# Optimization experiments

Hardware: AMD Instinct MI355X
Metric: run time of the kernel (lower is better)

The kernel has to match this reference:

```python
import jax, jax.numpy as jnp
import numpy as np

N = 100000
E = 3200000
NFEAT, NHID, NCLASS = 256, 128, 40


def setup_inputs() -> dict:
    key = jax.random.key(0)
    ks = jax.random.split(key, 8)
    return {
        "x": jax.random.normal(ks[0], (N, NFEAT), dtype=jnp.float32),
        "edge_src": jax.random.randint(ks[1], (E,), 0, N, dtype=jnp.int32),
        "edge_dst": jax.random.randint(ks[2], (E,), 0, N, dtype=jnp.int32),
        "edge_w": jax.random.uniform(ks[3], (E,), dtype=jnp.float32),
        "W0": jax.random.normal(ks[4], (NFEAT, NHID), dtype=jnp.float32) * (2.0 / (NFEAT + NHID)) ** 0.5,
        "b0": jax.random.normal(ks[5], (1, NHID), dtype=jnp.float32) * 0.1,
        "W1": jax.random.normal(ks[6], (NHID, NCLASS), dtype=jnp.float32) * (2.0 / (NHID + NCLASS)) ** 0.5,
        "b1": jax.random.normal(ks[7], (1, NCLASS), dtype=jnp.float32) * 0.1,
    }


def _l2_normalize(h, eps=1e-12):
    # F.normalize(x, p=2, dim=1)
    nrm = jnp.sqrt(jnp.sum(h * h, axis=1, keepdims=True))
    return h / jnp.maximum(nrm, eps)


def reference(x, edge_src, edge_dst, edge_w, W0, b0, W1, b1):
    n_nodes = x.shape[0]

    def spmm(h):  # adj @ h with edge-list sparse adjacency
        return jax.ops.segment_sum(edge_w[:, None] * h[edge_src], edge_dst, num_segments=n_nodes)

    # layer 1: GraphConvolution = spmm(x @ W) + bias (dropout is identity in eval)
    h = spmm(x @ W0) + b0
    h = _l2_normalize(h)        # atg.Z1
    h = jax.nn.relu(h)          # atg.H1
    # layer 2
    z = spmm(h @ W1) + b1       # atg.Z2
    return jax.nn.log_softmax(z, axis=1)
```

## Files before the change

### kernel.cpp

```cpp
#include <hip/hip_runtime.h>
#include <math.h>

#define NN 100000
#define NE 3200000
#define NF 256
#define NH 128
#define NC 40

#define CH 8192
#define NBLK 391
#define NBUCK 782
#define HTOT (NBUCK * NBLK)
#define HS1 ((HTOT + 511) / 512)
#define NTILE 1563

typedef unsigned int uint;
typedef short short8 __attribute__((ext_vector_type(8)));
typedef float floatx4 __attribute__((ext_vector_type(4)));

__device__ __forceinline__ float bflo(uint v) { return __uint_as_float(v << 16); }
__device__ __forceinline__ float bfhi(uint v) { return __uint_as_float(v & 0xffff0000u); }
__device__ __forceinline__ unsigned short f2bf(float f) {
    const uint u = __float_as_uint(f);
    return (unsigned short)((u + 0x7fffu + ((u >> 16) & 1u)) >> 16);
}
__device__ __forceinline__ uint pack2bf(float a, float b) {
    return (uint)f2bf(a) | ((uint)f2bf(b) << 16);
}

union ABfrag { uint u[4]; short8 s; };

__global__ __launch_bounds__(256) void w0pack_k(const float* __restrict__ W0,
                                                uint4* __restrict__ W0p) {
    const int idx = blockIdx.x * 256 + threadIdx.x;
    if (idx >= 4096) return;
    const int lane  = idx & 63;
    const int ntile = (idx >> 6) & 7;
    const int kstep = idx >> 9;
    const int n  = ntile * 16 + (lane & 15);
    const int kb = kstep * 32 + (lane >> 4) * 8;
    uint w[4];
#pragma unroll
    for (int ww = 0; ww < 4; ++ww)
        w[ww] = pack2bf(W0[(size_t)(kb + 2 * ww) * NH + n],
                        W0[(size_t)(kb + 2 * ww + 1) * NH + n]);
    W0p[idx] = make_uint4(w[0], w[1], w[2], w[3]);
}

__global__ __launch_bounds__(256) void gemm1_mfma(const float* __restrict__ x,
                                                  const uint4* __restrict__ W0p,
                                                  unsigned short* __restrict__ xwh) {
    __shared__ __align__(16) uint4 sB[4096];
    for (int i = threadIdx.x; i < 4096; i += 256) sB[i] = W0p[i];
    __syncthreads();

    const int wave = threadIdx.x >> 6;
    const int lane = threadIdx.x & 63;
    const int quad = lane >> 4;
    const int mcol = lane & 15;

    for (int tile = blockIdx.x; tile < NTILE; tile += 512) {
        const int row  = tile * 64 + wave * 16 + mcol;
        const int rowc = min(row, NN - 1);
        const float* xr = x + (size_t)rowc * NF + quad * 8;

        floatx4 acc[8] = {};
        float4 lo = *(const float4*)(xr);
        float4 hi = *(const float4*)(xr + 4);
#pragma unroll
        for (int ks = 0; ks < 8; ++ks) {
            ABfrag a;
            a.u[0] = pack2bf(lo.x, lo.y);
            a.u[1] = pack2bf(lo.z, lo.w);
            a.u[2] = pack2bf(hi.x, hi.y);
            a.u[3] = pack2bf(hi.z, hi.w);
            if (ks < 7) {
                lo = *(const float4*)(xr + (ks + 1) * 32);
                hi = *(const float4*)(xr + (ks + 1) * 32 + 4);
            }
#pragma unroll
            for (int nt = 0; nt < 8; ++nt) {
                ABfrag b;
                const uint4 bw = sB[(ks * 8 + nt) * 64 + lane];
                b.u[0] = bw.x; b.u[1] = bw.y; b.u[2] = bw.z; b.u[3] = bw.w;
                acc[nt] = __builtin_amdgcn_mfma_f32_16x16x32_bf16(a.s, b.s, acc[nt], 0, 0, 0);
            }
        }
        const int rowbase = tile * 64 + wave * 16 + quad * 4;
#pragma unroll
        for (int nt = 0; nt < 8; ++nt) {
#pragma unroll
            for (int r = 0; r < 4; ++r) {
                const int rr = rowbase + r;
                if (rr < NN) xwh[(size_t)rr * NH + nt * 16 + mcol] = f2bf(acc[nt][r]);
            }
        }
    }
}

__global__ __launch_bounds__(256) void p1hist_k(const int* __restrict__ edst,
                                                int* __restrict__ hmat) {
    __shared__ uint h[NBUCK];
    for (int i = threadIdx.x; i < NBUCK; i += 256) h[i] = 0;
    __syncthreads();
    const int b = blockIdx.x;
    const int e0 = b * CH, e1 = min(NE, e0 + CH);
    for (int e = e0 + threadIdx.x; e < e1; e += 256)
        atomicAdd(&h[((uint)edst[e]) >> 7], 1u);
    __syncthreads();
    for (int i = threadIdx.x; i < NBUCK; i += 256)
        hmat[(size_t)i * NBLK + b] = (int)h[i];
}

__global__ __launch_bounds__(512) void hscan1_k(int* __restrict__ hmat,
                                                int* __restrict__ partials) {
    __shared__ int s[512];
    const int t = threadIdx.x;
    const int i = blockIdx.x * 512 + t;
    const int v = (i < HTOT) ? hmat[i] : 0;
    s[t] = v;
    __syncthreads();
#pragma unroll
    for (int off = 1; off < 512; off <<= 1) {
        int a = (t >= off) ? s[t - off] : 0;
        __syncthreads();
        s[t] += a;
        __syncthreads();
    }
    if (i < HTOT) hmat[i] = s[t] - v;
    if (t == 511) partials[blockIdx.x] = s[t];
}

__global__ __launch_bounds__(1024) void hscan2_k(int* __restrict__ partials, int nb) {
    __shared__ int s[1024];
    const int t = threadIdx.x;
    const int v = (t < nb) ? partials[t] : 0;
    s[t] = v;
    __syncthreads();
#pragma unroll
    for (int off = 1; off < 1024; off <<= 1) {
        int a = (t >= off) ? s[t - off] : 0;
        __syncthreads();
        s[t] += a;
        __syncthreads();
    }
    if (t < nb) partials[t] = s[t] - v;
}

__global__ __launch_bounds__(512) void hscan3_k(int* __restrict__ hmat,
                                                const int* __restrict__ partials) {
    const int i = blockIdx.x * 512 + threadIdx.x;
    if (i < HTOT) hmat[i] += partials[blockIdx.x];
}

__global__ __launch_bounds__(256) void p1scat_k(const int* __restrict__ esrc,
                                                const int* __restrict__ edst,
                                                const float* __restrict__ ew,
                                                const int* __restrict__ hmat,
                                                uint2* __restrict__ ep1) {
    __shared__ uint base[NBUCK];
    const int b = blockIdx.x;
    for (int i = threadIdx.x; i < NBUCK; i += 256)
        base[i] = (uint)hmat[(size_t)i * NBLK + b];
    __syncthreads();
    const int e0 = b * CH, e1 = min(NE, e0 + CH);
    for (int e = e0 + threadIdx.x; e < e1; e += 256) {
        const uint d = (uint)edst[e];
        const uint pos = atomicAdd(&base[d >> 7], 1u);
        ep1[pos] = make_uint2((uint)esrc[e] | ((d & 127u) << 17), __float_as_uint(ew[e]));
    }
}

__global__ __launch_bounds__(256) void p2_k(const int* __restrict__ hmat,
                                            const uint2* __restrict__ ep1,
                                            uint2* __restrict__ ep,
                                            int* __restrict__ rp) {
    const int bk = blockIdx.x;
    const int beg = hmat[(size_t)bk * NBLK];
    const int end = (bk == NBUCK - 1) ? NE : hmat[(size_t)(bk + 1) * NBLK];
    __shared__ uint cnt[128];
    __shared__ uint st[128];
    if (threadIdx.x < 128) cnt[threadIdx.x] = 0;
    __syncthreads();
    for (int j = beg + threadIdx.x; j < end; j += 256)
        atomicAdd(&cnt[(ep1[j].x >> 17) & 127u], 1u);
    __syncthreads();
    if (threadIdx.x < 128) st[threadIdx.x] = cnt[threadIdx.x];
    __syncthreads();
#pragma unroll
    for (int off = 1; off < 128; off <<= 1) {
        uint a = 0;
        if (threadIdx.x < 128 && threadIdx.x >= off) a = st[threadIdx.x - off];
        __syncthreads();
        if (threadIdx.x < 128) st[threadIdx.x] += a;
        __syncthreads();
    }
    if (threadIdx.x < 128) {
        const uint start = st[threadIdx.x] - cnt[threadIdx.x];
        const int d = bk * 128 + threadIdx.x;
        if (d < NN) rp[d] = beg + (int)start;
        cnt[threadIdx.x] = (uint)beg + start;
    }
    if (bk == 0 && threadIdx.x == 200) rp[NN] = NE;
    __syncthreads();
    for (int j = beg + threadIdx.x; j < end; j += 256) {
        const uint2 r = ep1[j];
        const uint pos = atomicAdd(&cnt[(r.x >> 17) & 127u], 1u);
        ep[pos] = r;
    }
}

__global__ __launch_bounds__(256) void spmm1n_g(const int* __restrict__ rp,
                                                const uint2* __restrict__ ep,
                                                const uint* __restrict__ xwb,
                                                const float* __restrict__ b0,
                                                uint* __restrict__ h2b) {
    const int n = blockIdx.x * 4 + (threadIdx.x >> 6);
    const int t = threadIdx.x & 63;
    const int beg = rp[n], end = rp[n + 1];
    float a0 = 0.f, a1 = 0.f;
    int j = beg;
    for (; j + 7 < end; j += 8) {
        uint2 e[8];
        uint v[8];
#pragma unroll
        for (int u = 0; u < 8; ++u) e[u] = ep[j + u];
#pragma unroll
        for (int u = 0; u < 8; ++u) v[u] = xwb[(size_t)(e[u].x & 0x1FFFFu) * 64 + t];
#pragma unroll
        for (int u = 0; u < 8; ++u) {
            const float w = __uint_as_float(e[u].y);
            a0 = fmaf(w, bflo(v[u]), a0);
            a1 = fmaf(w, bfhi(v[u]), a1);
        }
    }
    for (; j < end; ++j) {
        const uint2 e = ep[j];
        const uint v = xwb[(size_t)(e.x & 0x1FFFFu) * 64 + t];
        const float w = __uint_as_float(e.y);
        a0 = fmaf(w, bflo(v), a0); a1 = fmaf(w, bfhi(v), a1);
    }
    const float2 bb = *(const float2*)(b0 + 2 * t);
    const float v0 = a0 + bb.x, v1 = a1 + bb.y;
    float s = v0 * v0 + v1 * v1;
#pragma unroll
    for (int o = 1; o < 64; o <<= 1) s += __shfl_xor(s, o, 64);
    const float scale = 1.0f / fmaxf(sqrtf(s), 1e-12f);
    h2b[(size_t)n * 64 + t] = pack2bf(fmaxf(v0 * scale, 0.0f), fmaxf(v1 * scale, 0.0f));
}

__global__ void gemm2_k(const uint* __restrict__ h2b,
                        const float* __restrict__ W1,
                        unsigned short* __restrict__ hwh) {
    __shared__ float sW1[NH * NC];
    const int lt = threadIdx.y * NC + threadIdx.x;
    for (int i = lt; i < NH * NC; i += 240) sW1[i] = W1[i];
    __syncthreads();
    const int n = blockIdx.x * 6 + threadIdx.y;
    if (n >= NN) return;
    const int f = threadIdx.x;
    const uint* hr = h2b + (size_t)n * 64;
    float acc = 0.f;
#pragma unroll 4
    for (int k8 = 0; k8 < 16; ++k8) {
        const uint4 hv = *(const uint4*)(hr + k8 * 4);
        const int kb = k8 * 8;
        acc = fmaf(bflo(hv.x), sW1[(kb + 0) * NC + f], acc);
        acc = fmaf(bfhi(hv.x), sW1[(kb + 1) * NC + f], acc);
        acc = fmaf(bflo(hv.y), sW1[(kb + 2) * NC + f], acc);
        acc = fmaf(bfhi(hv.y), sW1[(kb + 3) * NC + f], acc);
        acc = fmaf(bflo(hv.z), sW1[(kb + 4) * NC + f], acc);
        acc = fmaf(bfhi(hv.z), sW1[(kb + 5) * NC + f], acc);
        acc = fmaf(bflo(hv.w), sW1[(kb + 6) * NC + f], acc);
        acc = fmaf(bfhi(hv.w), sW1[(kb + 7) * NC + f], acc);
    }
    hwh[(size_t)n * NC + f] = f2bf(acc);
}

__global__ __launch_bounds__(320) void spmm2l_g(const int* __restrict__ rp,
                                                const uint2* __restrict__ ep,
                                                const uint* __restrict__ hwb,
                                                const float* __restrict__ b1,
                                                float2* __restrict__ out2) {
    const int nl = threadIdx.x / 20;
    const int g  = threadIdx.x % 20;
    const int n  = blockIdx.x * 16 + nl;
    const int beg = rp[n], end = rp[n + 1];
    float a0 = 0.f, a1 = 0.f;
    int j = beg;
    for (; j + 7 < end; j += 8) {
        uint2 e[8];
        uint v[8];
#pragma unroll
        for (int u = 0; u < 8; ++u) e[u] = ep[j + u];
#pragma unroll
        for (int u = 0; u < 8; ++u) v[u] = hwb[(size_t)(e[u].x & 0x1FFFFu) * 20 + g];
#pragma unroll
        for (int u = 0; u < 8; ++u) {
            const float w = __uint_as_float(e[u].y);
            a0 = fmaf(w, bflo(v[u]), a0);
            a1 = fmaf(w, bfhi(v[u]), a1);
        }
    }
    for (; j < end; ++j) {
        const uint2 e = ep[j];
        const uint v = hwb[(size_t)(e.x & 0x1FFFFu) * 20 + g];
        const float w = __uint_as_float(e.y);
        a0 = fmaf(w, bflo(v), a0); a1 = fmaf(w, bfhi(v), a1);
    }
    const float2 bb = *(const float2*)(b1 + 2 * g);
    a0 += bb.x; a1 += bb.y;
    __shared__ float red[16 * 20];
    __shared__ float stat[16];
    red[nl * 20 + g] = fmaxf(a0, a1);
    __syncthreads();
    if (g == 0) {
        float m = -INFINITY;
#pragma unroll
        for (int q = 0; q < 20; ++q) m = fmaxf(m, red[nl * 20 + q]);
        stat[nl] = m;
    }
    __syncthreads();
    const float m = stat[nl];
    red[nl * 20 + g] = expf(a0 - m) + expf(a1 - m);
    __syncthreads();
    if (g == 0) {
        float ssum = 0.f;
#pragma unroll
        for (int q = 0; q < 20; ++q) ssum += red[nl * 20 + q];
        stat[nl] = logf(ssum);
    }
    __syncthreads();
    const float lse = stat[nl];
    out2[(size_t)n * 20 + g] = make_float2(a0 - m - lse, a1 - m - lse);
}

extern "C" void kernel_launch(void* const* d_in, const int* in_sizes, int n_in,
                              void* d_out, int out_size, void* d_ws, size_t ws_size,
                              hipStream_t stream) {
    const float* x    = (const float*)d_in[0];
    const int*   esrc = (const int*)d_in[1];
    const int*   edst = (const int*)d_in[2];
    const float* ew   = (const float*)d_in[3];
    const float* W0   = (const float*)d_in[4];
    const float* b0   = (const float*)d_in[5];
    const float* W1   = (const float*)d_in[6];
    const float* b1   = (const float*)d_in[7];
    float* out = (float*)d_out;

    size_t o = 0;
    uint*  xwb  = (uint*)d_ws + o;  o += (size_t)NN * 64;
    uint*  h2b  = (uint*)d_ws + o;  o += (size_t)NN * 64;
    uint2* ep1  = (uint2*)h2b;
    uint*  hwb  = (uint*)d_ws + o;  o += (size_t)NN * 20;
    uint2* ep   = (uint2*)((uint*)d_ws + o); o += (size_t)NE * 2;
    int*   hmat = (int*)d_ws + o;   o += HTOT;
    int*   rp   = (int*)d_ws + o;   o += NN + 2;
    int*   partials = (int*)d_ws + o; o += 1024;
    if (o & 3) o += 4 - (o & 3);
    uint4* W0p  = (uint4*)((uint*)d_ws + o); o += 16384;

    w0pack_k<<<16, 256, 0, stream>>>(W0, W0p);
    gemm1_mfma<<<512, 256, 0, stream>>>(x, W0p, (unsigned short*)xwb);

    p1hist_k<<<NBLK, 256, 0, stream>>>(edst, hmat);
    hscan1_k<<<HS1, 512, 0, stream>>>(hmat, partials);
    hscan2_k<<<1, 1024, 0, stream>>>(partials, HS1);
    hscan3_k<<<HS1, 512, 0, stream>>>(hmat, partials);
    p1scat_k<<<NBLK, 256, 0, stream>>>(esrc, edst, ew, hmat, ep1);
    p2_k<<<NBUCK, 256, 0, stream>>>(hmat, ep1, ep, rp);

    spmm1n_g<<<NN / 4, 256, 0, stream>>>(rp, ep, xwb, b0, h2b);
    gemm2_k<<<(NN + 5) / 6, dim3(40, 6), 0, stream>>>(h2b, W1, (unsigned short*)hwb);
    spmm2l_g<<<NN / 16, 320, 0, stream>>>(rp, ep, hwb, b1, (float2*)out);
}
```

Measured before the change: 580.4 us.

## Use MFMA for second GEMM, fold scan fixup, vectorize histogram, scalarize edge loads

Replaces the scalar FMA gemm2 with a bf16 MFMA kernel that uses a W1 panel pre-packed and zero-padded to 48 columns, with the packing fused into the W0 pack kernel. Drops the hscan3 fixup kernel and instead adds the block partials directly where p1scat and p2 read hmat. Vectorizes the histogram edge loads to int4. In spmm1 it broadcasts the edge src and weight through readfirstlane so they sit in scalar registers. Together these cut kernel launches, ALU work and VGPR pressure. The int4 histogram loop assumes the chunk size divides evenly, which holds for CH=8192 and NE.

```diff
diff --git a/kernel.cpp b/kernel.cpp
--- a/kernel.cpp
+++ b/kernel.cpp
@@ -30,21 +30,39 @@
 
 union ABfrag { uint u[4]; short8 s; };
 
-__global__ __launch_bounds__(256) void w0pack_k(const float* __restrict__ W0,
-                                                uint4* __restrict__ W0p) {
+__global__ __launch_bounds__(256) void prep_pack_k(const float* __restrict__ W0,
+                                                   const float* __restrict__ W1,
+                                                   uint4* __restrict__ W0p,
+                                                   uint4* __restrict__ W1p) {
     const int idx = blockIdx.x * 256 + threadIdx.x;
-    if (idx >= 4096) return;
-    const int lane  = idx & 63;
-    const int ntile = (idx >> 6) & 7;
-    const int kstep = idx >> 9;
-    const int n  = ntile * 16 + (lane & 15);
-    const int kb = kstep * 32 + (lane >> 4) * 8;
-    uint w[4];
-#pragma unroll
-    for (int ww = 0; ww < 4; ++ww)
-        w[ww] = pack2bf(W0[(size_t)(kb + 2 * ww) * NH + n],
-                        W0[(size_t)(kb + 2 * ww + 1) * NH + n]);
-    W0p[idx] = make_uint4(w[0], w[1], w[2], w[3]);
+    if (idx < 4096) {
+        const int lane  = idx & 63;
+        const int ntile = (idx >> 6) & 7;
+        const int kstep = idx >> 9;
+        const int n  = ntile * 16 + (lane & 15);
+        const int kb = kstep * 32 + (lane >> 4) * 8;
+        uint w[4];
+#pragma unroll
+        for (int ww = 0; ww < 4; ++ww)
+            w[ww] = pack2bf(W0[(size_t)(kb + 2 * ww) * NH + n],
+                            W0[(size_t)(kb + 2 * ww + 1) * NH + n]);
+        W0p[idx] = make_uint4(w[0], w[1], w[2], w[3]);
+    } else if (idx < 4096 + 768) {
+        const int i2 = idx - 4096;
+        const int lane  = i2 & 63;
+        const int ntile = (i2 >> 6) % 3;
+        const int kstep = (i2 >> 6) / 3;
+        const int n  = ntile * 16 + (lane & 15);
+        const int kb = kstep * 32 + (lane >> 4) * 8;
+        uint w[4];
+#pragma unroll
+        for (int ww = 0; ww < 4; ++ww) {
+            const float lo = (n < NC) ? W1[(size_t)(kb + 2 * ww) * NC + n] : 0.0f;
+            const float hi = (n < NC) ? W1[(size_t)(kb + 2 * ww + 1) * NC + n] : 0.0f;
+            w[ww] = pack2bf(lo, hi);
+        }
+        W1p[i2] = make_uint4(w[0], w[1], w[2], w[3]);
+    }
 }
 
 __global__ __launch_bounds__(256) void gemm1_mfma(const float* __restrict__ x,
@@ -105,8 +123,13 @@
     __syncthreads();
     const int b = blockIdx.x;
     const int e0 = b * CH, e1 = min(NE, e0 + CH);
-    for (int e = e0 + threadIdx.x; e < e1; e += 256)
-        atomicAdd(&h[((uint)edst[e]) >> 7], 1u);
+    for (int e = e0 + threadIdx.x * 4; e + 3 < e1; e += 1024) {
+        const int4 d4 = *(const int4*)(edst + e);
+        atomicAdd(&h[((uint)d4.x) >> 7], 1u);
+        atomicAdd(&h[((uint)d4.y) >> 7], 1u);
+        atomicAdd(&h[((uint)d4.z) >> 7], 1u);
+        atomicAdd(&h[((uint)d4.w) >> 7], 1u);
+    }
     __syncthreads();
     for (int i = threadIdx.x; i < NBUCK; i += 256)
         hmat[(size_t)i * NBLK + b] = (int)h[i];
@@ -147,21 +170,18 @@
     if (t < nb) partials[t] = s[t] - v;
 }
 
-__global__ __launch_bounds__(512) void hscan3_k(int* __restrict__ hmat,
-                                                const int* __restrict__ partials) {
-    const int i = blockIdx.x * 512 + threadIdx.x;
-    if (i < HTOT) hmat[i] += partials[blockIdx.x];
-}
-
 __global__ __launch_bounds__(256) void p1scat_k(const int* __restrict__ esrc,
                                                 const int* __restrict__ edst,
                                                 const float* __restrict__ ew,
                                                 const int* __restrict__ hmat,
+                                                const int* __restrict__ partials,
                                                 uint2* __restrict__ ep1) {
     __shared__ uint base[NBUCK];
     const int b = blockIdx.x;
-    for (int i = threadIdx.x; i < NBUCK; i += 256)
-        base[i] = (uint)hmat[(size_t)i * NBLK + b];
+    for (int i = threadIdx.x; i < NBUCK; i += 256) {
+        const int g = i * NBLK + b;
+        base[i] = (uint)(hmat[g] + partials[g >> 9]);
+    }
     __syncthreads();
     const int e0 = b * CH, e1 = min(NE, e0 + CH);
     for (int e = e0 + threadIdx.x; e < e1; e += 256) {
@@ -172,12 +192,16 @@
 }
 
 __global__ __launch_bounds__(256) void p2_k(const int* __restrict__ hmat,
+                                            const int* __restrict__ partials,
                                             const uint2* __restrict__ ep1,
                                             uint2* __restrict__ ep,
                                             int* __restrict__ rp) {
     const int bk = blockIdx.x;
-    const int beg = hmat[(size_t)bk * NBLK];
-    const int end = (bk == NBUCK - 1) ? NE : hmat[(size_t)(bk + 1) * NBLK];
+    const int gb = bk * NBLK;
+    const int beg = hmat[gb] + partials[gb >> 9];
+    int end;
+    if (bk == NBUCK - 1) end = NE;
+    else { const int ge = gb + NBLK; end = hmat[ge] + partials[ge >> 9]; }
     __shared__ uint cnt[128];
     __shared__ uint st[128];
     if (threadIdx.x < 128) cnt[threadIdx.x] = 0;
@@ -217,27 +241,33 @@
                                                 uint* __restrict__ h2b) {
     const int n = blockIdx.x * 4 + (threadIdx.x >> 6);
     const int t = threadIdx.x & 63;
-    const int beg = rp[n], end = rp[n + 1];
+    const int beg = __builtin_amdgcn_readfirstlane(rp[n]);
+    const int end = __builtin_amdgcn_readfirstlane(rp[n + 1]);
     float a0 = 0.f, a1 = 0.f;
     int j = beg;
     for (; j + 7 < end; j += 8) {
-        uint2 e[8];
+        uint sx[8];
+        float w[8];
+#pragma unroll
+        for (int u = 0; u < 8; ++u) {
+            const uint2 e = ep[j + u];
+            sx[u] = __builtin_amdgcn_readfirstlane(e.x) & 0x1FFFFu;
+            w[u]  = __uint_as_float(__builtin_amdgcn_readfirstlane(e.y));
+        }
         uint v[8];
 #pragma unroll
-        for (int u = 0; u < 8; ++u) e[u] = ep[j + u];
-#pragma unroll
-        for (int u = 0; u < 8; ++u) v[u] = xwb[(size_t)(e[u].x & 0x1FFFFu) * 64 + t];
+        for (int u = 0; u < 8; ++u) v[u] = xwb[(size_t)sx[u] * 64 + t];
 #pragma unroll
         for (int u = 0; u < 8; ++u) {
-            const float w = __uint_as_float(e[u].y);
-            a0 = fmaf(w, bflo(v[u]), a0);
-            a1 = fmaf(w, bfhi(v[u]), a1);
+            a0 = fmaf(w[u], bflo(v[u]), a0);
+            a1 = fmaf(w[u], bfhi(v[u]), a1);
         }
     }
     for (; j < end; ++j) {
         const uint2 e = ep[j];
-        const uint v = xwb[(size_t)(e.x & 0x1FFFFu) * 64 + t];
-        const float w = __uint_as_float(e.y);
+        const uint sx = __builtin_amdgcn_readfirstlane(e.x) & 0x1FFFFu;
+        const float w = __uint_as_float(__builtin_amdgcn_readfirstlane(e.y));
+        const uint v = xwb[(size_t)sx * 64 + t];
         a0 = fmaf(w, bflo(v), a0); a1 = fmaf(w, bfhi(v), a1);
     }
     const float2 bb = *(const float2*)(b0 + 2 * t);
@@ -249,32 +279,47 @@
     h2b[(size_t)n * 64 + t] = pack2bf(fmaxf(v0 * scale, 0.0f), fmaxf(v1 * scale, 0.0f));
 }
 
-__global__ void gemm2_k(const uint* __restrict__ h2b,
-                        const float* __restrict__ W1,
-                        unsigned short* __restrict__ hwh) {
-    __shared__ float sW1[NH * NC];
-    const int lt = threadIdx.y * NC + threadIdx.x;
-    for (int i = lt; i < NH * NC; i += 240) sW1[i] = W1[i];
-    __syncthreads();
-    const int n = blockIdx.x * 6 + threadIdx.y;
-    if (n >= NN) return;
-    const int f = threadIdx.x;
-    const uint* hr = h2b + (size_t)n * 64;
-    float acc = 0.f;
-#pragma unroll 4
-    for (int k8 = 0; k8 < 16; ++k8) {
-        const uint4 hv = *(const uint4*)(hr + k8 * 4);
-        const int kb = k8 * 8;
-        acc = fmaf(bflo(hv.x), sW1[(kb + 0) * NC + f], acc);
-        acc = fmaf(bfhi(hv.x), sW1[(kb + 1) * NC + f], acc);
-        acc = fmaf(bflo(hv.y), sW1[(kb + 2) * NC + f], acc);
-        acc = fmaf(bfhi(hv.y), sW1[(kb + 3) * NC + f], acc);
-        acc = fmaf(bflo(hv.z), sW1[(kb + 4) * NC + f], acc);
-        acc = fmaf(bfhi(hv.z), sW1[(kb + 5) * NC + f], acc);
-        acc = fmaf(bflo(hv.w), sW1[(kb + 6) * NC + f], acc);
-        acc = fmaf(bfhi(hv.w), sW1[(kb + 7) * NC + f], acc);
-    }
-    hwh[(size_t)n * NC + f] = f2bf(acc);
+__global__ __launch_bounds__(256) void gemm2_mfma(const uint* __restrict__ h2b,
+                                                  const uint4* __restrict__ W1p,
+                                                  unsigned short* __restrict__ hwh) {
+    __shared__ __align__(16) uint4 sB[768];
+    for (int i = threadIdx.x; i < 768; i += 256) sB[i] = W1p[i];
+    __syncthreads();
+
+    const int wave = threadIdx.x >> 6;
+    const int lane = threadIdx.x & 63;
+    const int quad = lane >> 4;
+    const int mcol = lane & 15;
+    const int row  = blockIdx.x * 64 + wave * 16 + mcol;
+    const int rowc = min(row, NN - 1);
+    const uint* hr = h2b + (size_t)rowc * 64;
+
+    floatx4 acc[3] = {};
+#pragma unroll
+    for (int ks = 0; ks < 4; ++ks) {
+        ABfrag a;
+        const uint4 hv = *(const uint4*)(hr + ks * 16 + quad * 4);
+        a.u[0] = hv.x; a.u[1] = hv.y; a.u[2] = hv.z; a.u[3] = hv.w;
+#pragma unroll
+        for (int nt = 0; nt < 3; ++nt) {
+            ABfrag b;
+            const uint4 bw = sB[(ks * 3 + nt) * 64 + lane];
+            b.u[0] = bw.x; b.u[1] = bw.y; b.u[2] = bw.z; b.u[3] = bw.w;
+            acc[nt] = __builtin_amdgcn_mfma_f32_16x16x32_bf16(a.s, b.s, acc[nt], 0, 0, 0);
+        }
+    }
+    const int rowbase = blockIdx.x * 64 + wave * 16 + quad * 4;
+#pragma unroll
+    for (int nt = 0; nt < 3; ++nt) {
+        const int f = nt * 16 + mcol;
+        if (f < NC) {
+#pragma unroll
+            for (int r = 0; r < 4; ++r) {
+                const int rr = rowbase + r;
+                if (rr < NN) hwh[(size_t)rr * NC + f] = f2bf(acc[nt][r]);
+            }
+        }
+    }
 }
 
 __global__ __launch_bounds__(320) void spmm2l_g(const int* __restrict__ rp,
@@ -359,18 +404,18 @@
     int*   partials = (int*)d_ws + o; o += 1024;
     if (o & 3) o += 4 - (o & 3);
     uint4* W0p  = (uint4*)((uint*)d_ws + o); o += 16384;
-
-    w0pack_k<<<16, 256, 0, stream>>>(W0, W0p);
+    uint4* W1p  = (uint4*)((uint*)d_ws + o); o += 3072;
+
+    prep_pack_k<<<19, 256, 0, stream>>>(W0, W1, W0p, W1p);
     gemm1_mfma<<<512, 256, 0, stream>>>(x, W0p, (unsigned short*)xwb);
 
     p1hist_k<<<NBLK, 256, 0, stream>>>(edst, hmat);
     hscan1_k<<<HS1, 512, 0, stream>>>(hmat, partials);
     hscan2_k<<<1, 1024, 0, stream>>>(partials, HS1);
-    hscan3_k<<<HS1, 512, 0, stream>>>(hmat, partials);
-    p1scat_k<<<NBLK, 256, 0, stream>>>(esrc, edst, ew, hmat, ep1);
-    p2_k<<<NBUCK, 256, 0, stream>>>(hmat, ep1, ep, rp);
+    p1scat_k<<<NBLK, 256, 0, stream>>>(esrc, edst, ew, hmat, partials, ep1);
+    p2_k<<<NBUCK, 256, 0, stream>>>(hmat, partials, ep1, ep, rp);
 
     spmm1n_g<<<NN / 4, 256, 0, stream>>>(rp, ep, xwb, b0, h2b);
-    gemm2_k<<<(NN + 5) / 6, dim3(40, 6), 0, stream>>>(h2b, W1, (unsigned short*)hwb);
+    gemm2_mfma<<<NTILE, 256, 0, stream>>>(h2b, W1p, (unsigned short*)hwb);
     spmm2l_g<<<NN / 16, 320, 0, stream>>>(rp, ep, hwb, b1, (float2*)out);
 }
```

Result: faster. 514.1 us (-11.4%).
